# Optimization experiments

Measured on AMD Instinct MI355X. Metric: run time of the kernel, lower is better.

## Reference

```python
import jax, jax.numpy as jnp
import numpy as np

N_VOX = 50000   # number of voxels
M_VIEW = 12     # multiview features per voxel
F_DIM = 256     # vision feature dim
N_CAM = 48      # number of cameras
B = 16384       # batch of query voxel indices
H = 8           # num_heads
DK = 64         # dim_key
DV = 64         # dim_value
PE_ORDER = 8    # positional-encoding order -> spatial dim = 3*PE_ORDER
SIGMA = 1.0


def spatial_encode(x):
    # SpatialEncoder(3, pe_order, 1.0): sinusoidal PE producing pe_order*3 features.
    # freqs = sigma * 2^i, i in [0, pe_order)
    freqs = SIGMA * (2.0 ** jnp.arange(PE_ORDER, dtype=x.dtype))  # (P,)
    # x: (B, 3) -> (B, P, 3) -> (B, P*3)
    return jnp.sin(x[:, None, :] * freqs[None, :, None]).reshape(x.shape[0], PE_ORDER * 3)


def setup_inputs() -> dict:
    key = jax.random.key(0)
    ks = jax.random.split(key, 9)
    vox_indices = jax.random.randint(ks[0], (B,), 0, N_VOX)
    voxels = jax.random.normal(ks[1], (N_VOX, 3), dtype=jnp.float32) * 2.0
    voxel_features = jax.random.normal(ks[2], (N_VOX, M_VIEW, F_DIM), dtype=jnp.float32)
    scores = jax.random.normal(ks[3], (N_VOX, M_VIEW), dtype=jnp.float32)
    # ensure each voxel has at least one valid view so the masked softmax is finite
    scores = scores.at[:, 0].set(jnp.abs(scores[:, 0]))
    camera_ids = jax.random.randint(ks[4], (N_VOX, M_VIEW), 0, N_CAM)
    extrinsics = jax.random.normal(ks[5], (N_CAM, 16), dtype=jnp.float32)
    W_q = jax.random.normal(ks[6], (PE_ORDER * 3, DK * H), dtype=jnp.float32) * 0.05
    W_k = jax.random.normal(ks[7], (F_DIM + 16, DK * H), dtype=jnp.float32) * 0.05
    W_v = jax.random.normal(ks[8], (F_DIM, DV * H), dtype=jnp.float32) * 0.05
    return dict(vox_indices=vox_indices, voxels=voxels, voxel_features=voxel_features,
                voxel_feature_scores=scores, camera_ids=camera_ids, extrinsics=extrinsics,
                W_q=W_q, W_k=W_k, W_v=W_v)


def reference(vox_indices, voxels, voxel_features, voxel_feature_scores,
              camera_ids, extrinsics, W_q, W_k, W_v):
    # --- query path: gather xyz, normalize, PE, project ---
    vmin = jnp.min(voxels, axis=0)
    vmax = jnp.max(voxels, axis=0)
    vox_xyzs = (voxels[vox_indices] - vmin) / (vmax - vmin) - 0.5          # (B, 3)
    pe = spatial_encode(vox_xyzs)                                          # (B, 3P)
    query = (pe @ W_q).reshape(B, H, DK)                                   # (B, H, DK)

    # --- key/value path: gather multiview features + extrinsics ---
    vox_feats = voxel_features[vox_indices]                                # (B, M, F)
    value = (vox_feats @ W_v).reshape(B, M_VIEW, H, DV)                    # (B, M, H, DV)
    cam = camera_ids[vox_indices]                                          # (B, M)
    ext = extrinsics[cam]                                                  # (B, M, 16)
    aug = jnp.concatenate([vox_feats, ext], axis=-1)                       # (B, M, F+16)
    k = (aug @ W_k).reshape(B, M_VIEW, H, DK)                              # (B, M, H, DK)

    # --- additive mask from scores ---
    scores = voxel_feature_scores[vox_indices]                             # (B, M)
    mask = jnp.where(scores < 0, -jnp.inf, 0.0).astype(query.dtype)        # (B, M)

    # --- single-query masked cross attention ---
    logits = jnp.einsum('bhd,bmhd->bhm', query, k) / np.sqrt(DK) + mask[:, None, :]
    p = jax.nn.softmax(logits, axis=-1)                                    # (B, H, M)
    attn = jnp.einsum('bhm,bmhd->bhd', p, value)                           # (B, H, DV)
    return attn.reshape(B, H * DV)
```

## Files before the change

### kernel.cpp

```cpp
#include <hip/hip_runtime.h>
#include <math.h>

#define NVOX 50000
#define MV   12
#define FD   256
#define AUGD 272
#define BQ   16384
#define HN   8
#define DKC  64
#define HD   512
#define PEO  8
#define G    4

__global__ void kmm_part(const float* __restrict__ vox, float* __restrict__ part) {
    int tid = threadIdx.x;
    float mn[3] = {1e30f, 1e30f, 1e30f};
    float mx[3] = {-1e30f, -1e30f, -1e30f};
    for (int i = blockIdx.x * 256 + tid; i < NVOX; i += 64 * 256) {
        #pragma unroll
        for (int c = 0; c < 3; ++c) {
            float v = vox[3 * i + c];
            mn[c] = fminf(mn[c], v);
            mx[c] = fmaxf(mx[c], v);
        }
    }
    #pragma unroll
    for (int s = 1; s < 64; s <<= 1) {
        #pragma unroll
        for (int c = 0; c < 3; ++c) {
            mn[c] = fminf(mn[c], __shfl_xor(mn[c], s, 64));
            mx[c] = fmaxf(mx[c], __shfl_xor(mx[c], s, 64));
        }
    }
    __shared__ float smn[4][3], smx[4][3];
    int w = tid >> 6;
    if ((tid & 63) == 0) {
        #pragma unroll
        for (int c = 0; c < 3; ++c) { smn[w][c] = mn[c]; smx[w][c] = mx[c]; }
    }
    __syncthreads();
    if (tid == 0) {
        #pragma unroll
        for (int c = 0; c < 3; ++c) {
            float a = fminf(fminf(smn[0][c], smn[1][c]), fminf(smn[2][c], smn[3][c]));
            float b = fmaxf(fmaxf(smx[0][c], smx[1][c]), fmaxf(smx[2][c], smx[3][c]));
            part[blockIdx.x * 6 + c] = a;
            part[blockIdx.x * 6 + 3 + c] = b;
        }
    }
}

__global__ void kmm_final(const float* __restrict__ part, float* __restrict__ mm) {
    int t = threadIdx.x;
    float mn[3], mx[3];
    #pragma unroll
    for (int c = 0; c < 3; ++c) { mn[c] = part[t * 6 + c]; mx[c] = part[t * 6 + 3 + c]; }
    #pragma unroll
    for (int s = 1; s < 64; s <<= 1) {
        #pragma unroll
        for (int c = 0; c < 3; ++c) {
            mn[c] = fminf(mn[c], __shfl_xor(mn[c], s, 64));
            mx[c] = fmaxf(mx[c], __shfl_xor(mx[c], s, 64));
        }
    }
    if (t == 0) {
        #pragma unroll
        for (int c = 0; c < 3; ++c) { mm[c] = mn[c]; mm[3 + c] = mx[c]; }
    }
}

__global__ __launch_bounds__(256) void kattn(
    const int* __restrict__ vi, const float* __restrict__ voxels,
    const float* __restrict__ feats, const float* __restrict__ scores,
    const int* __restrict__ cams, const float* __restrict__ extr,
    const float* __restrict__ Wq, const float* __restrict__ Wk, const float* __restrict__ Wv,
    const float* __restrict__ mm, float* __restrict__ out)
{
    __shared__ float q_s[G][HN][68];
    __shared__ float qWpf[G][HN][280];
    __shared__ float lp_s[G][MV][HN];
    __shared__ float ext_s[G][MV][16];
    __shared__ float pe_s[G][24];
    __shared__ float mask_s[G][MV];

    const int tid = threadIdx.x;
    const int b0 = blockIdx.x * G;

    if (tid < G * 24) {
        int g = tid / 24, t = tid % 24;
        int idx = vi[b0 + g];
        int p = t / 3, c = t % 3;
        float vmn = mm[c], vmx = mm[3 + c];
        float x = (voxels[idx * 3 + c] - vmn) / (vmx - vmn) - 0.5f;
        pe_s[g][t] = sinf(x * (float)(1 << p));
    }
    if (tid < G * MV) {
        int g = tid / MV, m = tid % MV;
        int idx = vi[b0 + g];
        mask_s[g][m] = (scores[idx * MV + m] < 0.0f) ? -1e30f : 0.0f;
    }
    for (int e = tid; e < G * MV * 16; e += 256) {
        int g = e / (MV * 16), r = e % (MV * 16);
        int m = r >> 4, c = r & 15;
        int idx = vi[b0 + g];
        int cam = cams[idx * MV + m];
        ext_s[g][m][c] = extr[cam * 16 + c];
    }
    __syncthreads();

    {
        const float2* Wq2 = (const float2*)Wq;
        float2 w[24];
        #pragma unroll
        for (int t = 0; t < 24; ++t) w[t] = Wq2[t * 256 + tid];
        int h = tid >> 5, d2 = (tid & 31) * 2;
        #pragma unroll
        for (int g = 0; g < G; ++g) {
            float q0 = 0.f, q1 = 0.f;
            #pragma unroll
            for (int t = 0; t < 24; ++t) {
                float p = pe_s[g][t];
                q0 = fmaf(p, w[t].x, q0);
                q1 = fmaf(p, w[t].y, q1);
            }
            *(float2*)&q_s[g][h][d2] = make_float2(q0, q1);
        }
    }
    __syncthreads();

    {
        int h = tid & 7, tq = tid >> 3;
        for (int pass = 0; pass < 3; ++pass) {
            int tbase = (pass * 32 + tq) * 4;
            if (tbase < AUGD) {
                float acc[G][4];
                #pragma unroll
                for (int g = 0; g < G; ++g)
                    #pragma unroll
                    for (int r = 0; r < 4; ++r) acc[g][r] = 0.f;
                const float* wkb = Wk + (size_t)tbase * HD + h * 64;
                #pragma unroll 4
                for (int d4 = 0; d4 < 16; ++d4) {
                    float4 wk0 = *(const float4*)(wkb + 0 * HD + d4 * 4);
                    float4 wk1 = *(const float4*)(wkb + 1 * HD + d4 * 4);
                    float4 wk2 = *(const float4*)(wkb + 2 * HD + d4 * 4);
                    float4 wk3 = *(const float4*)(wkb + 3 * HD + d4 * 4);
                    #pragma unroll
                    for (int g = 0; g < G; ++g) {
                        float4 qv = *(const float4*)&q_s[g][h][d4 * 4];
                        acc[g][0] += qv.x*wk0.x + qv.y*wk0.y + qv.z*wk0.z + qv.w*wk0.w;
                        acc[g][1] += qv.x*wk1.x + qv.y*wk1.y + qv.z*wk1.z + qv.w*wk1.w;
                        acc[g][2] += qv.x*wk2.x + qv.y*wk2.y + qv.z*wk2.z + qv.w*wk2.w;
                        acc[g][3] += qv.x*wk3.x + qv.y*wk3.y + qv.z*wk3.z + qv.w*wk3.w;
                    }
                }
                #pragma unroll
                for (int g = 0; g < G; ++g)
                    *(float4*)&qWpf[g][h][tbase] =
                        make_float4(acc[g][0], acc[g][1], acc[g][2], acc[g][3]);
            }
        }
    }
    __syncthreads();

    {
        #pragma unroll
        for (int k = 0; k < 3; ++k) {
            int id = tid + k * 256;
            int half = id & 1;
            int h = (id >> 1) & 7;
            int gm = id >> 4;
            int m = gm % MV;
            int g = gm / MV;
            int idx = vi[b0 + g];
            const float4* fr = (const float4*)(feats + (size_t)idx * (MV * FD) + m * FD);
            const float4* qw = (const float4*)&qWpf[g][h][0];
            const float4* fr4 = fr + half * 32;
            const float4* qw4 = qw + half * 32;
            float acc = 0.f;
            #pragma unroll 8
            for (int i = 0; i < 32; ++i) {
                float4 f = fr4[i];
                float4 w = qw4[i];
                acc += f.x*w.x + f.y*w.y + f.z*w.z + f.w*w.w;
            }
            if (half) {
                const float4* er = (const float4*)&ext_s[g][m][0];
                #pragma unroll
                for (int e4 = 0; e4 < 4; ++e4) {
                    float4 f = er[e4];
                    float4 w = qw[64 + e4];
                    acc += f.x*w.x + f.y*w.y + f.z*w.z + f.w*w.w;
                }
            }
            acc += __shfl_xor(acc, 1, 64);
            if (half == 0) lp_s[g][m][h] = acc * 0.125f + mask_s[g][m];
        }
    }
    __syncthreads();

    if (tid < G * HN) {
        int g = tid >> 3, h = tid & 7;
        float l[MV], mx = -1e30f;
        #pragma unroll
        for (int m = 0; m < MV; ++m) { l[m] = lp_s[g][m][h]; mx = fmaxf(mx, l[m]); }
        float s = 0.f;
        #pragma unroll
        for (int m = 0; m < MV; ++m) { l[m] = __expf(l[m] - mx); s += l[m]; }
        float inv = 1.0f / s;
        #pragma unroll
        for (int m = 0; m < MV; ++m) lp_s[g][m][h] = l[m] * inv;
    }
    __syncthreads();

    {
        int g = tid >> 6, to = tid & 63;
        int idx = vi[b0 + g];
        const float4* fr = (const float4*)(feats + (size_t)idx * (MV * FD));
        float acc[HN][4];
        #pragma unroll
        for (int h = 0; h < HN; ++h)
            #pragma unroll
            for (int r = 0; r < 4; ++r) acc[h][r] = 0.f;
        #pragma unroll 4
        for (int m = 0; m < MV; ++m) {
            float4 f  = fr[m * 64 + to];
            float4 p0 = *(const float4*)&lp_s[g][m][0];
            float4 p1 = *(const float4*)&lp_s[g][m][4];
            acc[0][0] = fmaf(p0.x, f.x, acc[0][0]); acc[0][1] = fmaf(p0.x, f.y, acc[0][1]);
            acc[0][2] = fmaf(p0.x, f.z, acc[0][2]); acc[0][3] = fmaf(p0.x, f.w, acc[0][3]);
            acc[1][0] = fmaf(p0.y, f.x, acc[1][0]); acc[1][1] = fmaf(p0.y, f.y, acc[1][1]);
            acc[1][2] = fmaf(p0.y, f.z, acc[1][2]); acc[1][3] = fmaf(p0.y, f.w, acc[1][3]);
            acc[2][0] = fmaf(p0.z, f.x, acc[2][0]); acc[2][1] = fmaf(p0.z, f.y, acc[2][1]);
            acc[2][2] = fmaf(p0.z, f.z, acc[2][2]); acc[2][3] = fmaf(p0.z, f.w, acc[2][3]);
            acc[3][0] = fmaf(p0.w, f.x, acc[3][0]); acc[3][1] = fmaf(p0.w, f.y, acc[3][1]);
            acc[3][2] = fmaf(p0.w, f.z, acc[3][2]); acc[3][3] = fmaf(p0.w, f.w, acc[3][3]);
            acc[4][0] = fmaf(p1.x, f.x, acc[4][0]); acc[4][1] = fmaf(p1.x, f.y, acc[4][1]);
            acc[4][2] = fmaf(p1.x, f.z, acc[4][2]); acc[4][3] = fmaf(p1.x, f.w, acc[4][3]);
            acc[5][0] = fmaf(p1.y, f.x, acc[5][0]); acc[5][1] = fmaf(p1.y, f.y, acc[5][1]);
            acc[5][2] = fmaf(p1.y, f.z, acc[5][2]); acc[5][3] = fmaf(p1.y, f.w, acc[5][3]);
            acc[6][0] = fmaf(p1.z, f.x, acc[6][0]); acc[6][1] = fmaf(p1.z, f.y, acc[6][1]);
            acc[6][2] = fmaf(p1.z, f.z, acc[6][2]); acc[6][3] = fmaf(p1.z, f.w, acc[6][3]);
            acc[7][0] = fmaf(p1.w, f.x, acc[7][0]); acc[7][1] = fmaf(p1.w, f.y, acc[7][1]);
            acc[7][2] = fmaf(p1.w, f.z, acc[7][2]); acc[7][3] = fmaf(p1.w, f.w, acc[7][3]);
        }
        #pragma unroll
        for (int h = 0; h < HN; ++h)
            *(float4*)&qWpf[g][h][to * 4] =
                make_float4(acc[h][0], acc[h][1], acc[h][2], acc[h][3]);
    }
    __syncthreads();

    {
        const float2* Wv2 = (const float2*)Wv;
        int h = tid >> 5;
        float o[G][2];
        #pragma unroll
        for (int g = 0; g < G; ++g) { o[g][0] = 0.f; o[g][1] = 0.f; }
        #pragma unroll 4
        for (int t4 = 0; t4 < 64; ++t4) {
            float2 w0 = Wv2[(t4 * 4 + 0) * 256 + tid];
            float2 w1 = Wv2[(t4 * 4 + 1) * 256 + tid];
            float2 w2 = Wv2[(t4 * 4 + 2) * 256 + tid];
            float2 w3 = Wv2[(t4 * 4 + 3) * 256 + tid];
            #pragma unroll
            for (int g = 0; g < G; ++g) {
                float4 pf = *(const float4*)&qWpf[g][h][t4 * 4];
                o[g][0] = fmaf(pf.x, w0.x, o[g][0]); o[g][0] = fmaf(pf.y, w1.x, o[g][0]);
                o[g][0] = fmaf(pf.z, w2.x, o[g][0]); o[g][0] = fmaf(pf.w, w3.x, o[g][0]);
                o[g][1] = fmaf(pf.x, w0.y, o[g][1]); o[g][1] = fmaf(pf.y, w1.y, o[g][1]);
                o[g][1] = fmaf(pf.z, w2.y, o[g][1]); o[g][1] = fmaf(pf.w, w3.y, o[g][1]);
            }
        }
        #pragma unroll
        for (int g = 0; g < G; ++g)
            ((float2*)out)[(size_t)(b0 + g) * (HD / 2) + tid] = make_float2(o[g][0], o[g][1]);
    }
}

extern "C" void kernel_launch(void* const* d_in, const int* in_sizes, int n_in,
                              void* d_out, int out_size, void* d_ws, size_t ws_size,
                              hipStream_t stream) {
    const int*   vi      = (const int*)d_in[0];
    const float* voxels  = (const float*)d_in[1];
    const float* feats   = (const float*)d_in[2];
    const float* scores  = (const float*)d_in[3];
    const int*   cams    = (const int*)d_in[4];
    const float* extr    = (const float*)d_in[5];
    const float* Wq      = (const float*)d_in[6];
    const float* Wk      = (const float*)d_in[7];
    const float* Wv      = (const float*)d_in[8];
    float* out = (float*)d_out;

    float* ws   = (float*)d_ws;
    float* mm   = ws;
    float* part = ws + 8;

    kmm_part<<<64, 256, 0, stream>>>(voxels, part);
    kmm_final<<<1, 64, 0, stream>>>(part, mm);
    kattn<<<BQ / G, 256, 0, stream>>>(vi, voxels, feats, scores, cams, extr, Wq, Wk, Wv, mm, out);
}
```

Measured before the change: 1.262 ms.

## Fuse query-key projection into logit computation, keep qWk in registers

Restructures the logit stage so each wavefront computes q·Wk for two heads directly into registers, then combines it with the gathered features and extrinsics through wave-wide shuffle reductions. This removes the qWpf shared-memory round trip and one barrier. Shared memory is aliased into a smaller buffer, and launch bounds request 4 blocks per CU to raise occupancy. The trade-off is more shuffle reductions (24 values over 6 steps per g) and higher register pressure.

```diff
diff --git a/kernel.cpp b/kernel.cpp
--- a/kernel.cpp
+++ b/kernel.cpp
@@ -11,6 +11,7 @@
 #define HD   512
 #define PEO  8
 #define G    4
+#define PFS  260
 
 __global__ void kmm_part(const float* __restrict__ vox, float* __restrict__ part) {
     int tid = threadIdx.x;
@@ -69,42 +70,49 @@
     }
 }
 
-__global__ __launch_bounds__(256) void kattn(
+__global__ __launch_bounds__(256, 4) void kattn(
     const int* __restrict__ vi, const float* __restrict__ voxels,
     const float* __restrict__ feats, const float* __restrict__ scores,
     const int* __restrict__ cams, const float* __restrict__ extr,
     const float* __restrict__ Wq, const float* __restrict__ Wk, const float* __restrict__ Wv,
     const float* __restrict__ mm, float* __restrict__ out)
 {
-    __shared__ float q_s[G][HN][68];
-    __shared__ float qWpf[G][HN][280];
-    __shared__ float lp_s[G][MV][HN];
-    __shared__ float ext_s[G][MV][16];
-    __shared__ float pe_s[G][24];
+    __shared__ __align__(16) float smem[G * HN * PFS];
+    __shared__ __align__(16) float lgt_s[G][HN][12];
+    __shared__ __align__(16) float p_s[G][MV][8];
     __shared__ float mask_s[G][MV];
+
+    float* pf    = smem;
+    float* ext_s = smem;
+    float* pe_s  = smem + G * MV * 16;
+    float* q_s   = smem + G * MV * 16 + G * 24;
+    #define EXT(g,m,e) ext_s[(((g)*MV + (m)) << 4) + (e)]
+    #define QS(g,h,d)  q_s[(((g)*HN + (h)) << 6) + (d)]
+    #define PFE(g,h,t) pf[((g)*HN + (h)) * PFS + (t)]
 
     const int tid = threadIdx.x;
     const int b0 = blockIdx.x * G;
 
+    int idxs[G];
+    #pragma unroll
+    for (int g = 0; g < G; ++g) idxs[g] = vi[b0 + g];
+
     if (tid < G * 24) {
         int g = tid / 24, t = tid % 24;
-        int idx = vi[b0 + g];
         int p = t / 3, c = t % 3;
         float vmn = mm[c], vmx = mm[3 + c];
-        float x = (voxels[idx * 3 + c] - vmn) / (vmx - vmn) - 0.5f;
-        pe_s[g][t] = sinf(x * (float)(1 << p));
+        float x = (voxels[idxs[g] * 3 + c] - vmn) / (vmx - vmn) - 0.5f;
+        pe_s[g * 24 + t] = sinf(x * (float)(1 << p));
     }
     if (tid < G * MV) {
         int g = tid / MV, m = tid % MV;
-        int idx = vi[b0 + g];
-        mask_s[g][m] = (scores[idx * MV + m] < 0.0f) ? -1e30f : 0.0f;
+        mask_s[g][m] = (scores[idxs[g] * MV + m] < 0.0f) ? -1e30f : 0.0f;
     }
     for (int e = tid; e < G * MV * 16; e += 256) {
         int g = e / (MV * 16), r = e % (MV * 16);
         int m = r >> 4, c = r & 15;
-        int idx = vi[b0 + g];
-        int cam = cams[idx * MV + m];
-        ext_s[g][m][c] = extr[cam * 16 + c];
+        int cam = cams[idxs[g] * MV + m];
+        EXT(g, m, c) = extr[cam * 16 + c];
     }
     __syncthreads();
 
@@ -113,88 +121,117 @@
         float2 w[24];
         #pragma unroll
         for (int t = 0; t < 24; ++t) w[t] = Wq2[t * 256 + tid];
-        int h = tid >> 5, d2 = (tid & 31) * 2;
+        int h = tid >> 5, c2 = (tid & 31) * 2;
         #pragma unroll
         for (int g = 0; g < G; ++g) {
             float q0 = 0.f, q1 = 0.f;
             #pragma unroll
             for (int t = 0; t < 24; ++t) {
-                float p = pe_s[g][t];
+                float p = pe_s[g * 24 + t];
                 q0 = fmaf(p, w[t].x, q0);
                 q1 = fmaf(p, w[t].y, q1);
             }
-            *(float2*)&q_s[g][h][d2] = make_float2(q0, q1);
-        }
-    }
-    __syncthreads();
+            *(float2*)&QS(g, h, c2) = make_float2(q0, q1);
+        }
+    }
 
     {
-        int h = tid & 7, tq = tid >> 3;
-        for (int pass = 0; pass < 3; ++pass) {
-            int tbase = (pass * 32 + tq) * 4;
-            if (tbase < AUGD) {
-                float acc[G][4];
-                #pragma unroll
-                for (int g = 0; g < G; ++g)
-                    #pragma unroll
-                    for (int r = 0; r < 4; ++r) acc[g][r] = 0.f;
-                const float* wkb = Wk + (size_t)tbase * HD + h * 64;
-                #pragma unroll 4
-                for (int d4 = 0; d4 < 16; ++d4) {
-                    float4 wk0 = *(const float4*)(wkb + 0 * HD + d4 * 4);
-                    float4 wk1 = *(const float4*)(wkb + 1 * HD + d4 * 4);
-                    float4 wk2 = *(const float4*)(wkb + 2 * HD + d4 * 4);
-                    float4 wk3 = *(const float4*)(wkb + 3 * HD + d4 * 4);
+        const int wv = tid >> 6, l = tid & 63;
+        const int h0 = 2 * wv;
+
+        float qk[2][4][G];
+        #pragma unroll
+        for (int hh = 0; hh < 2; ++hh)
+            #pragma unroll
+            for (int r = 0; r < 4; ++r)
+                #pragma unroll
+                for (int g = 0; g < G; ++g) qk[hh][r][g] = 0.f;
+
+        const float* wkbase = Wk + (size_t)(4 * l) * HD;
+        #pragma unroll
+        for (int hh = 0; hh < 2; ++hh) {
+            const float* wkh = wkbase + (h0 + hh) * 64;
+            #pragma unroll
+            for (int d8 = 0; d8 < 8; ++d8) {
+                float4 qa[G], qb[G];
+                #pragma unroll
+                for (int g = 0; g < G; ++g) {
+                    qa[g] = *(const float4*)&QS(g, h0 + hh, d8 * 8);
+                    qb[g] = *(const float4*)&QS(g, h0 + hh, d8 * 8 + 4);
+                }
+                #pragma unroll
+                for (int r = 0; r < 4; ++r) {
+                    float4 wa = *(const float4*)(wkh + r * HD + d8 * 8);
+                    float4 wb = *(const float4*)(wkh + r * HD + d8 * 8 + 4);
                     #pragma unroll
                     for (int g = 0; g < G; ++g) {
-                        float4 qv = *(const float4*)&q_s[g][h][d4 * 4];
-                        acc[g][0] += qv.x*wk0.x + qv.y*wk0.y + qv.z*wk0.z + qv.w*wk0.w;
-                        acc[g][1] += qv.x*wk1.x + qv.y*wk1.y + qv.z*wk1.z + qv.w*wk1.w;
-                        acc[g][2] += qv.x*wk2.x + qv.y*wk2.y + qv.z*wk2.z + qv.w*wk2.w;
-                        acc[g][3] += qv.x*wk3.x + qv.y*wk3.y + qv.z*wk3.z + qv.w*wk3.w;
+                        qk[hh][r][g] += qa[g].x * wa.x + qa[g].y * wa.y
+                                      + qa[g].z * wa.z + qa[g].w * wa.w
+                                      + qb[g].x * wb.x + qb[g].y * wb.y
+                                      + qb[g].z * wb.z + qb[g].w * wb.w;
                     }
                 }
-                #pragma unroll
-                for (int g = 0; g < G; ++g)
-                    *(float4*)&qWpf[g][h][tbase] =
-                        make_float4(acc[g][0], acc[g][1], acc[g][2], acc[g][3]);
-            }
-        }
-    }
-    __syncthreads();
-
-    {
-        #pragma unroll
-        for (int k = 0; k < 3; ++k) {
-            int id = tid + k * 256;
-            int half = id & 1;
-            int h = (id >> 1) & 7;
-            int gm = id >> 4;
-            int m = gm % MV;
-            int g = gm / MV;
-            int idx = vi[b0 + g];
-            const float4* fr = (const float4*)(feats + (size_t)idx * (MV * FD) + m * FD);
-            const float4* qw = (const float4*)&qWpf[g][h][0];
-            const float4* fr4 = fr + half * 32;
-            const float4* qw4 = qw + half * 32;
-            float acc = 0.f;
-            #pragma unroll 8
-            for (int i = 0; i < 32; ++i) {
-                float4 f = fr4[i];
-                float4 w = qw4[i];
-                acc += f.x*w.x + f.y*w.y + f.z*w.z + f.w*w.w;
-            }
-            if (half) {
-                const float4* er = (const float4*)&ext_s[g][m][0];
-                #pragma unroll
-                for (int e4 = 0; e4 < 4; ++e4) {
-                    float4 f = er[e4];
-                    float4 w = qw[64 + e4];
-                    acc += f.x*w.x + f.y*w.y + f.z*w.z + f.w*w.w;
+            }
+        }
+
+        const int tr  = l & 15;
+        const int thh = (l >> 4) & 1;
+        const int tdh = l >> 5;
+        float qkt0[G], qkt1[G];
+        {
+            const float* wkt = Wk + (size_t)(256 + tr) * HD + (h0 + thh) * 64 + tdh * 32;
+            float acc[G] = {0.f, 0.f, 0.f, 0.f};
+            #pragma unroll
+            for (int d8 = 0; d8 < 4; ++d8) {
+                float4 wa = *(const float4*)(wkt + d8 * 8);
+                float4 wb = *(const float4*)(wkt + d8 * 8 + 4);
+                #pragma unroll
+                for (int g = 0; g < G; ++g) {
+                    float4 qa = *(const float4*)&QS(g, h0 + thh, tdh * 32 + d8 * 8);
+                    float4 qb = *(const float4*)&QS(g, h0 + thh, tdh * 32 + d8 * 8 + 4);
+                    acc[g] += qa.x * wa.x + qa.y * wa.y + qa.z * wa.z + qa.w * wa.w
+                            + qb.x * wb.x + qb.y * wb.y + qb.z * wb.z + qb.w * wb.w;
                 }
             }
-            acc += __shfl_xor(acc, 1, 64);
-            if (half == 0) lp_s[g][m][h] = acc * 0.125f + mask_s[g][m];
+            #pragma unroll
+            for (int g = 0; g < G; ++g) {
+                acc[g] += __shfl_xor(acc[g], 32, 64);
+                qkt0[g] = (l < 16) ? acc[g] : 0.f;
+                qkt1[g] = (l >= 16 && l < 32) ? acc[g] : 0.f;
+            }
+        }
+
+        #pragma unroll
+        for (int g = 0; g < G; ++g) {
+            const float4* fr = (const float4*)(feats + (size_t)idxs[g] * (MV * FD));
+            float part0[MV], part1[MV];
+            #pragma unroll
+            for (int m = 0; m < MV; ++m) {
+                float4 f = fr[m * 64 + l];
+                part0[m] = f.x * qk[0][0][g] + f.y * qk[0][1][g]
+                         + f.z * qk[0][2][g] + f.w * qk[0][3][g];
+                part1[m] = f.x * qk[1][0][g] + f.y * qk[1][1][g]
+                         + f.z * qk[1][2][g] + f.w * qk[1][3][g];
+                float e = EXT(g, m, tr);
+                part0[m] = fmaf(e, qkt0[g], part0[m]);
+                part1[m] = fmaf(e, qkt1[g], part1[m]);
+            }
+            #pragma unroll
+            for (int s = 1; s < 64; s <<= 1) {
+                #pragma unroll
+                for (int m = 0; m < MV; ++m) {
+                    part0[m] += __shfl_xor(part0[m], s, 64);
+                    part1[m] += __shfl_xor(part1[m], s, 64);
+                }
+            }
+            if (l == 0) {
+                *(float4*)&lgt_s[g][h0][0] = make_float4(part0[0], part0[1], part0[2], part0[3]);
+                *(float4*)&lgt_s[g][h0][4] = make_float4(part0[4], part0[5], part0[6], part0[7]);
+                *(float4*)&lgt_s[g][h0][8] = make_float4(part0[8], part0[9], part0[10], part0[11]);
+                *(float4*)&lgt_s[g][h0 + 1][0] = make_float4(part1[0], part1[1], part1[2], part1[3]);
+                *(float4*)&lgt_s[g][h0 + 1][4] = make_float4(part1[4], part1[5], part1[6], part1[7]);
+                *(float4*)&lgt_s[g][h0 + 1][8] = make_float4(part1[8], part1[9], part1[10], part1[11]);
+            }
         }
     }
     __syncthreads();
@@ -203,20 +240,22 @@
         int g = tid >> 3, h = tid & 7;
         float l[MV], mx = -1e30f;
         #pragma unroll
-        for (int m = 0; m < MV; ++m) { l[m] = lp_s[g][m][h]; mx = fmaxf(mx, l[m]); }
+        for (int m = 0; m < MV; ++m) {
+            l[m] = lgt_s[g][h][m] * 0.125f + mask_s[g][m];
+            mx = fmaxf(mx, l[m]);
+        }
         float s = 0.f;
         #pragma unroll
         for (int m = 0; m < MV; ++m) { l[m] = __expf(l[m] - mx); s += l[m]; }
         float inv = 1.0f / s;
         #pragma unroll
-        for (int m = 0; m < MV; ++m) lp_s[g][m][h] = l[m] * inv;
+        for (int m = 0; m < MV; ++m) p_s[g][m][h] = l[m] * inv;
     }
     __syncthreads();
 
     {
         int g = tid >> 6, to = tid & 63;
-        int idx = vi[b0 + g];
-        const float4* fr = (const float4*)(feats + (size_t)idx * (MV * FD));
+        const float4* fr = (const float4*)(feats + (size_t)idxs[g] * (MV * FD));
         float acc[HN][4];
         #pragma unroll
         for (int h = 0; h < HN; ++h)
@@ -225,8 +264,8 @@
         #pragma unroll 4
         for (int m = 0; m < MV; ++m) {
             float4 f  = fr[m * 64 + to];
-            float4 p0 = *(const float4*)&lp_s[g][m][0];
-            float4 p1 = *(const float4*)&lp_s[g][m][4];
+            float4 p0 = *(const float4*)&p_s[g][m][0];
+            float4 p1 = *(const float4*)&p_s[g][m][4];
             acc[0][0] = fmaf(p0.x, f.x, acc[0][0]); acc[0][1] = fmaf(p0.x, f.y, acc[0][1]);
             acc[0][2] = fmaf(p0.x, f.z, acc[0][2]); acc[0][3] = fmaf(p0.x, f.w, acc[0][3]);
             acc[1][0] = fmaf(p0.y, f.x, acc[1][0]); acc[1][1] = fmaf(p0.y, f.y, acc[1][1]);
@@ -244,9 +283,10 @@
             acc[7][0] = fmaf(p1.w, f.x, acc[7][0]); acc[7][1] = fmaf(p1.w, f.y, acc[7][1]);
             acc[7][2] = fmaf(p1.w, f.z, acc[7][2]); acc[7][3] = fmaf(p1.w, f.w, acc[7][3]);
         }
+        __syncthreads();
         #pragma unroll
         for (int h = 0; h < HN; ++h)
-            *(float4*)&qWpf[g][h][to * 4] =
+            *(float4*)&PFE(g, h, to * 4) =
                 make_float4(acc[h][0], acc[h][1], acc[h][2], acc[h][3]);
     }
     __syncthreads();
@@ -265,11 +305,11 @@
             float2 w3 = Wv2[(t4 * 4 + 3) * 256 + tid];
             #pragma unroll
             for (int g = 0; g < G; ++g) {
-                float4 pf = *(const float4*)&qWpf[g][h][t4 * 4];
-                o[g][0] = fmaf(pf.x, w0.x, o[g][0]); o[g][0] = fmaf(pf.y, w1.x, o[g][0]);
-                o[g][0] = fmaf(pf.z, w2.x, o[g][0]); o[g][0] = fmaf(pf.w, w3.x, o[g][0]);
-                o[g][1] = fmaf(pf.x, w0.y, o[g][1]); o[g][1] = fmaf(pf.y, w1.y, o[g][1]);
-                o[g][1] = fmaf(pf.z, w2.y, o[g][1]); o[g][1] = fmaf(pf.w, w3.y, o[g][1]);
+                float4 pfv = *(const float4*)&PFE(g, h, t4 * 4);
+                o[g][0] = fmaf(pfv.x, w0.x, o[g][0]); o[g][0] = fmaf(pfv.y, w1.x, o[g][0]);
+                o[g][0] = fmaf(pfv.z, w2.x, o[g][0]); o[g][0] = fmaf(pfv.w, w3.x, o[g][0]);
+                o[g][1] = fmaf(pfv.x, w0.y, o[g][1]); o[g][1] = fmaf(pfv.y, w1.y, o[g][1]);
+                o[g][1] = fmaf(pfv.z, w2.y, o[g][1]); o[g][1] = fmaf(pfv.w, w3.y, o[g][1]);
             }
         }
         #pragma unroll
```

Result: slower. 3.999 ms (+217.0%).
